# Performance work log

Hardware: AMD Instinct MI355X
Metric: run time of the kernel (lower is better)

Reference implementation:

```python
import jax, jax.numpy as jnp
import numpy as np

IN_FEATURES = 4096
OUT_FEATURES = 11008
BATCH = 2048


def setup_inputs() -> dict:
    key = jax.random.key(0)
    k1, k2, k3, k4 = jax.random.split(key, 4)
    # int8-range activations, stored as int32 for exact integer accumulation
    input = jax.random.randint(k1, (BATCH, IN_FEATURES), -127, 128, dtype=jnp.int32)
    # ternary weights in {-1, 0, 1}
    ternary_weight = jax.random.randint(k2, (OUT_FEATURES, IN_FEATURES), -1, 2, dtype=jnp.int32)
    weight_scale = jax.random.uniform(k3, (OUT_FEATURES, 1), dtype=jnp.float32, minval=0.01, maxval=0.1)
    bias = jax.random.normal(k4, (OUT_FEATURES,), dtype=jnp.float32) * 0.01
    return {"input": input, "ternary_weight": ternary_weight,
            "weight_scale": weight_scale, "bias": bias}


def reference(input, ternary_weight, weight_scale, bias):
    # Equivalent to the per-column add/sub loop: int32 accumulate of
    # input @ ternary_weight.T, since w in {-1,0,1}.
    acc = jnp.einsum('bi,oi->bo', input, ternary_weight)  # int32 [B, O]
    out = acc.astype(jnp.float32) * weight_scale.reshape(1, -1)
    out = out + bias
    return out
```

## Files before the change

### kernel.cpp

```cpp
#include <hip/hip_runtime.h>
#include <stdint.h>

#define BATCH   2048
#define KDIM    4096
#define NDIM    11008

#define BM 128
#define BN 256
#define BK 64
#define NT (KDIM / BK)
#define ABYTES (BM * BK)
#define BBYTES (BN * BK)
#define BUF_BYTES (ABYTES + BBYTES)
#define A_OFF 0
#define B_OFF ABYTES

typedef __attribute__((ext_vector_type(4))) int i32x4;

typedef const __attribute__((address_space(1))) char glob_char;
typedef __attribute__((address_space(3))) char lds_char;

__device__ __forceinline__ unsigned pack4(i32x4 v) {
  return  ((unsigned)v.x & 0xFFu)
        | (((unsigned)v.y & 0xFFu) << 8)
        | (((unsigned)v.z & 0xFFu) << 16)
        | (((unsigned)v.w)         << 24);
}

__global__ __launch_bounds__(256) void convert_i32_i8(const int* __restrict__ src,
                                                      unsigned* __restrict__ dst,
                                                      int n4) {
  int idx = blockIdx.x * 256 + threadIdx.x;
  if (idx >= n4) return;
  i32x4 v = ((const i32x4*)src)[idx];
  dst[idx] = pack4(v);
}

__global__ __launch_bounds__(256, 2) void ternary_gemm(const char* __restrict__ A8,
                                                       const char* __restrict__ B8,
                                                       const float* __restrict__ scale,
                                                       const float* __restrict__ bias,
                                                       float* __restrict__ out) {
  __shared__ char lds[3 * BUF_BYTES];

  const int tid  = threadIdx.x;
  const int wid  = tid >> 6;
  const int lane = tid & 63;

  const int nwg = gridDim.x;
  const int cpx = nwg >> 3;
  const int wg  = (blockIdx.x & 7) * cpx + (blockIdx.x >> 3);
  const int mt = wg & 15;
  const int nt = wg >> 4;
  const int arow0 = mt * BM;
  const int brow0 = nt * BN;

  const int wr = wid >> 1;
  const int wc = wid & 1;
  const int rsub = lane & 15;
  const int sgrp = lane >> 4;

  const int srow  = tid >> 2;
  const int sslot = (tid & 3) ^ ((srow >> 1) & 3);
  const char* gA0 = A8 + (size_t)(arow0       + srow) * KDIM + sslot * 16;
  const char* gA1 = A8 + (size_t)(arow0 +  64 + srow) * KDIM + sslot * 16;
  const char* gB0 = B8 + (size_t)(brow0       + srow) * KDIM + sslot * 16;
  const char* gB1 = B8 + (size_t)(brow0 +  64 + srow) * KDIM + sslot * 16;
  const char* gB2 = B8 + (size_t)(brow0 + 128 + srow) * KDIM + sslot * 16;
  const char* gB3 = B8 + (size_t)(brow0 + 192 + srow) * KDIM + sslot * 16;

  auto stage = [&](const char* g, int bufo, int kt, int dsto) {
    __builtin_amdgcn_global_load_lds((glob_char*)(g + kt * BK),
        (lds_char*)(lds + bufo + dsto + wid * 1024), 16, 0, 0);
  };

  int offA[4], offB[8];
#pragma unroll
  for (int m = 0; m < 4; ++m) {
    const int row = wr * 64 + m * 16 + rsub;
    const int p   = sgrp ^ ((row >> 1) & 3);
    offA[m] = A_OFF + row * 64 + p * 16;
  }
#pragma unroll
  for (int n = 0; n < 8; ++n) {
    const int row = wc * 128 + n * 16 + rsub;
    const int p   = sgrp ^ ((row >> 1) & 3);
    offB[n] = B_OFF + row * 64 + p * 16;
  }

  i32x4 acc[4][8];
#pragma unroll
  for (int m = 0; m < 4; ++m)
#pragma unroll
    for (int n = 0; n < 8; ++n)
      acc[m][n] = (i32x4){0, 0, 0, 0};

  int cur = 0, nxt = BUF_BYTES, pf = 2 * BUF_BYTES;

  stage(gB0, cur, 0, B_OFF);         stage(gB1, cur, 0, B_OFF + 4096);
  stage(gB2, cur, 0, B_OFF + 8192);  stage(gB3, cur, 0, B_OFF + 12288);
  stage(gA0, cur, 0, A_OFF);         stage(gA1, cur, 0, A_OFF + 4096);
  stage(gB0, nxt, 1, B_OFF);         stage(gB1, nxt, 1, B_OFF + 4096);
  stage(gB2, nxt, 1, B_OFF + 8192);  stage(gB3, nxt, 1, B_OFF + 12288);
  stage(gA0, nxt, 1, A_OFF);         stage(gA1, nxt, 1, A_OFF + 4096);
  asm volatile("s_waitcnt vmcnt(6)" ::: "memory");
  __builtin_amdgcn_s_barrier();

  for (int t = 0; t < NT; ++t) {
    const int kt2 = (t + 2 < NT) ? t + 2 : NT - 1;

    i32x4 a0, a1, a2, a3, b0, b1, b2, b3, b4, b5, b6, b7;

    a0 = *(const i32x4*)(lds + cur + offA[0]);
    a1 = *(const i32x4*)(lds + cur + offA[1]);
    b0 = *(const i32x4*)(lds + cur + offB[0]);
    b1 = *(const i32x4*)(lds + cur + offB[1]);
    b2 = *(const i32x4*)(lds + cur + offB[2]);
    b3 = *(const i32x4*)(lds + cur + offB[3]);
    stage(gB0, pf, kt2, B_OFF);
    stage(gB1, pf, kt2, B_OFF + 4096);
    __builtin_amdgcn_s_barrier();
    __builtin_amdgcn_s_setprio(1);
    acc[0][0] = __builtin_amdgcn_mfma_i32_16x16x64_i8(a0, b0, acc[0][0], 0, 0, 0);
    acc[0][1] = __builtin_amdgcn_mfma_i32_16x16x64_i8(a0, b1, acc[0][1], 0, 0, 0);
    acc[0][2] = __builtin_amdgcn_mfma_i32_16x16x64_i8(a0, b2, acc[0][2], 0, 0, 0);
    acc[0][3] = __builtin_amdgcn_mfma_i32_16x16x64_i8(a0, b3, acc[0][3], 0, 0, 0);
    acc[1][0] = __builtin_amdgcn_mfma_i32_16x16x64_i8(a1, b0, acc[1][0], 0, 0, 0);
    acc[1][1] = __builtin_amdgcn_mfma_i32_16x16x64_i8(a1, b1, acc[1][1], 0, 0, 0);
    acc[1][2] = __builtin_amdgcn_mfma_i32_16x16x64_i8(a1, b2, acc[1][2], 0, 0, 0);
    acc[1][3] = __builtin_amdgcn_mfma_i32_16x16x64_i8(a1, b3, acc[1][3], 0, 0, 0);
    __builtin_amdgcn_s_setprio(0);
    __builtin_amdgcn_s_barrier();

    b4 = *(const i32x4*)(lds + cur + offB[4]);
    b5 = *(const i32x4*)(lds + cur + offB[5]);
    b6 = *(const i32x4*)(lds + cur + offB[6]);
    b7 = *(const i32x4*)(lds + cur + offB[7]);
    stage(gB2, pf, kt2, B_OFF + 8192);
    stage(gB3, pf, kt2, B_OFF + 12288);
    __builtin_amdgcn_s_barrier();
    __builtin_amdgcn_s_setprio(1);
    acc[0][4] = __builtin_amdgcn_mfma_i32_16x16x64_i8(a0, b4, acc[0][4], 0, 0, 0);
    acc[0][5] = __builtin_amdgcn_mfma_i32_16x16x64_i8(a0, b5, acc[0][5], 0, 0, 0);
    acc[0][6] = __builtin_amdgcn_mfma_i32_16x16x64_i8(a0, b6, acc[0][6], 0, 0, 0);
    acc[0][7] = __builtin_amdgcn_mfma_i32_16x16x64_i8(a0, b7, acc[0][7], 0, 0, 0);
    acc[1][4] = __builtin_amdgcn_mfma_i32_16x16x64_i8(a1, b4, acc[1][4], 0, 0, 0);
    acc[1][5] = __builtin_amdgcn_mfma_i32_16x16x64_i8(a1, b5, acc[1][5], 0, 0, 0);
    acc[1][6] = __builtin_amdgcn_mfma_i32_16x16x64_i8(a1, b6, acc[1][6], 0, 0, 0);
    acc[1][7] = __builtin_amdgcn_mfma_i32_16x16x64_i8(a1, b7, acc[1][7], 0, 0, 0);
    __builtin_amdgcn_s_setprio(0);
    __builtin_amdgcn_s_barrier();

    a2 = *(const i32x4*)(lds + cur + offA[2]);
    a3 = *(const i32x4*)(lds + cur + offA[3]);
    stage(gA0, pf, kt2, A_OFF);
    stage(gA1, pf, kt2, A_OFF + 4096);
    __builtin_amdgcn_s_barrier();
    __builtin_amdgcn_s_setprio(1);
    acc[2][4] = __builtin_amdgcn_mfma_i32_16x16x64_i8(a2, b4, acc[2][4], 0, 0, 0);
    acc[2][5] = __builtin_amdgcn_mfma_i32_16x16x64_i8(a2, b5, acc[2][5], 0, 0, 0);
    acc[2][6] = __builtin_amdgcn_mfma_i32_16x16x64_i8(a2, b6, acc[2][6], 0, 0, 0);
    acc[2][7] = __builtin_amdgcn_mfma_i32_16x16x64_i8(a2, b7, acc[2][7], 0, 0, 0);
    acc[3][4] = __builtin_amdgcn_mfma_i32_16x16x64_i8(a3, b4, acc[3][4], 0, 0, 0);
    acc[3][5] = __builtin_amdgcn_mfma_i32_16x16x64_i8(a3, b5, acc[3][5], 0, 0, 0);
    acc[3][6] = __builtin_amdgcn_mfma_i32_16x16x64_i8(a3, b6, acc[3][6], 0, 0, 0);
    acc[3][7] = __builtin_amdgcn_mfma_i32_16x16x64_i8(a3, b7, acc[3][7], 0, 0, 0);
    __builtin_amdgcn_s_setprio(0);
    __builtin_amdgcn_s_barrier();

    asm volatile("s_waitcnt vmcnt(6)" ::: "memory");
    __builtin_amdgcn_s_barrier();
    __builtin_amdgcn_s_setprio(1);
    acc[2][0] = __builtin_amdgcn_mfma_i32_16x16x64_i8(a2, b0, acc[2][0], 0, 0, 0);
    acc[2][1] = __builtin_amdgcn_mfma_i32_16x16x64_i8(a2, b1, acc[2][1], 0, 0, 0);
    acc[2][2] = __builtin_amdgcn_mfma_i32_16x16x64_i8(a2, b2, acc[2][2], 0, 0, 0);
    acc[2][3] = __builtin_amdgcn_mfma_i32_16x16x64_i8(a2, b3, acc[2][3], 0, 0, 0);
    acc[3][0] = __builtin_amdgcn_mfma_i32_16x16x64_i8(a3, b0, acc[3][0], 0, 0, 0);
    acc[3][1] = __builtin_amdgcn_mfma_i32_16x16x64_i8(a3, b1, acc[3][1], 0, 0, 0);
    acc[3][2] = __builtin_amdgcn_mfma_i32_16x16x64_i8(a3, b2, acc[3][2], 0, 0, 0);
    acc[3][3] = __builtin_amdgcn_mfma_i32_16x16x64_i8(a3, b3, acc[3][3], 0, 0, 0);
    __builtin_amdgcn_s_setprio(0);
    __builtin_amdgcn_s_barrier();

    const int tb = cur; cur = nxt; nxt = pf; pf = tb;
  }

  const int crow = sgrp * 4;
#pragma unroll
  for (int n = 0; n < 8; ++n) {
    const int col = brow0 + wc * 128 + n * 16 + rsub;
    const float sc = scale[col];
    const float bs = bias[col];
#pragma unroll
    for (int m = 0; m < 4; ++m) {
      const int r0 = arow0 + wr * 64 + m * 16 + crow;
#pragma unroll
      for (int j = 0; j < 4; ++j) {
        out[(size_t)(r0 + j) * NDIM + col] = (float)acc[m][n][j] * sc + bs;
      }
    }
  }
}

extern "C" void kernel_launch(void* const* d_in, const int* in_sizes, int n_in,
                              void* d_out, int out_size, void* d_ws, size_t ws_size,
                              hipStream_t stream) {
  const int*   input  = (const int*)d_in[0];
  const int*   weight = (const int*)d_in[1];
  const float* scale  = (const float*)d_in[2];
  const float* bias   = (const float*)d_in[3];
  float*       out    = (float*)d_out;

  const size_t needA = (size_t)BATCH * KDIM;
  const size_t needB = (size_t)NDIM * KDIM;

  char* A8 = (char*)d_ws;
  char* B8 = A8 + needA;
  const int nA4 = (int)(needA / 4);
  const int nB4 = (int)(needB / 4);
  convert_i32_i8<<<(nA4 + 255) / 256, 256, 0, stream>>>(input, (unsigned*)A8, nA4);
  convert_i32_i8<<<(nB4 + 255) / 256, 256, 0, stream>>>(weight, (unsigned*)B8, nB4);

  const dim3 grid((BATCH / BM) * (NDIM / BN));
  const dim3 block(256);
  ternary_gemm<<<grid, block, 0, stream>>>(A8, B8, scale, bias, out);
  (void)ws_size; (void)n_in; (void)in_sizes; (void)out_size;
}
```

Measured before the change: 155.4 us.

## Flatten K-loop to single barrier phase and regroup workgroup tile mapping

```diff
diff --git a/kernel.cpp b/kernel.cpp
--- a/kernel.cpp
+++ b/kernel.cpp
@@ -47,11 +47,11 @@
   const int wid  = tid >> 6;
   const int lane = tid & 63;
 
-  const int nwg = gridDim.x;
-  const int cpx = nwg >> 3;
-  const int wg  = (blockIdx.x & 7) * cpx + (blockIdx.x >> 3);
-  const int mt = wg & 15;
-  const int nt = wg >> 4;
+  const int wg  = (blockIdx.x & 7) * 86 + (blockIdx.x >> 3);
+  const int mtq = wg / 172;
+  const int r   = wg - mtq * 172;
+  const int nt  = r >> 2;
+  const int mt  = mtq * 4 + (r & 3);
   const int arow0 = mt * BM;
   const int brow0 = nt * BN;
 
@@ -73,6 +73,14 @@
     __builtin_amdgcn_global_load_lds((glob_char*)(g + kt * BK),
         (lds_char*)(lds + bufo + dsto + wid * 1024), 16, 0, 0);
   };
+  auto stage_tile = [&](int bufo, int kt) {
+    stage(gA0, bufo, kt, A_OFF);
+    stage(gA1, bufo, kt, A_OFF + 4096);
+    stage(gB0, bufo, kt, B_OFF);
+    stage(gB1, bufo, kt, B_OFF + 4096);
+    stage(gB2, bufo, kt, B_OFF + 8192);
+    stage(gB3, bufo, kt, B_OFF + 12288);
+  };
 
   int offA[4], offB[8];
 #pragma unroll
@@ -97,89 +105,65 @@
 
   int cur = 0, nxt = BUF_BYTES, pf = 2 * BUF_BYTES;
 
-  stage(gB0, cur, 0, B_OFF);         stage(gB1, cur, 0, B_OFF + 4096);
-  stage(gB2, cur, 0, B_OFF + 8192);  stage(gB3, cur, 0, B_OFF + 12288);
-  stage(gA0, cur, 0, A_OFF);         stage(gA1, cur, 0, A_OFF + 4096);
-  stage(gB0, nxt, 1, B_OFF);         stage(gB1, nxt, 1, B_OFF + 4096);
-  stage(gB2, nxt, 1, B_OFF + 8192);  stage(gB3, nxt, 1, B_OFF + 12288);
-  stage(gA0, nxt, 1, A_OFF);         stage(gA1, nxt, 1, A_OFF + 4096);
+  stage_tile(cur, 0);
+  stage_tile(nxt, 1);
   asm volatile("s_waitcnt vmcnt(6)" ::: "memory");
   __builtin_amdgcn_s_barrier();
 
   for (int t = 0; t < NT; ++t) {
     const int kt2 = (t + 2 < NT) ? t + 2 : NT - 1;
 
-    i32x4 a0, a1, a2, a3, b0, b1, b2, b3, b4, b5, b6, b7;
-
-    a0 = *(const i32x4*)(lds + cur + offA[0]);
-    a1 = *(const i32x4*)(lds + cur + offA[1]);
-    b0 = *(const i32x4*)(lds + cur + offB[0]);
-    b1 = *(const i32x4*)(lds + cur + offB[1]);
-    b2 = *(const i32x4*)(lds + cur + offB[2]);
-    b3 = *(const i32x4*)(lds + cur + offB[3]);
-    stage(gB0, pf, kt2, B_OFF);
-    stage(gB1, pf, kt2, B_OFF + 4096);
-    __builtin_amdgcn_s_barrier();
+    stage_tile(pf, kt2);
+
+    i32x4 a0 = *(const i32x4*)(lds + cur + offA[0]);
+    i32x4 a1 = *(const i32x4*)(lds + cur + offA[1]);
+    i32x4 a2 = *(const i32x4*)(lds + cur + offA[2]);
+    i32x4 a3 = *(const i32x4*)(lds + cur + offA[3]);
+    i32x4 b0 = *(const i32x4*)(lds + cur + offB[0]);
+    i32x4 b1 = *(const i32x4*)(lds + cur + offB[1]);
+    i32x4 b2 = *(const i32x4*)(lds + cur + offB[2]);
+    i32x4 b3 = *(const i32x4*)(lds + cur + offB[3]);
+    i32x4 b4 = *(const i32x4*)(lds + cur + offB[4]);
+    i32x4 b5 = *(const i32x4*)(lds + cur + offB[5]);
+    i32x4 b6 = *(const i32x4*)(lds + cur + offB[6]);
+    i32x4 b7 = *(const i32x4*)(lds + cur + offB[7]);
+
     __builtin_amdgcn_s_setprio(1);
     acc[0][0] = __builtin_amdgcn_mfma_i32_16x16x64_i8(a0, b0, acc[0][0], 0, 0, 0);
+    acc[1][0] = __builtin_amdgcn_mfma_i32_16x16x64_i8(a1, b0, acc[1][0], 0, 0, 0);
+    acc[2][0] = __builtin_amdgcn_mfma_i32_16x16x64_i8(a2, b0, acc[2][0], 0, 0, 0);
+    acc[3][0] = __builtin_amdgcn_mfma_i32_16x16x64_i8(a3, b0, acc[3][0], 0, 0, 0);
     acc[0][1] = __builtin_amdgcn_mfma_i32_16x16x64_i8(a0, b1, acc[0][1], 0, 0, 0);
+    acc[1][1] = __builtin_amdgcn_mfma_i32_16x16x64_i8(a1, b1, acc[1][1], 0, 0, 0);
+    acc[2][1] = __builtin_amdgcn_mfma_i32_16x16x64_i8(a2, b1, acc[2][1], 0, 0, 0);
+    acc[3][1] = __builtin_amdgcn_mfma_i32_16x16x64_i8(a3, b1, acc[3][1], 0, 0, 0);
     acc[0][2] = __builtin_amdgcn_mfma_i32_16x16x64_i8(a0, b2, acc[0][2], 0, 0, 0);
+    acc[1][2] = __builtin_amdgcn_mfma_i32_16x16x64_i8(a1, b2, acc[1][2], 0, 0, 0);
+    acc[2][2] = __builtin_amdgcn_mfma_i32_16x16x64_i8(a2, b2, acc[2][2], 0, 0, 0);
+    acc[3][2] = __builtin_amdgcn_mfma_i32_16x16x64_i8(a3, b2, acc[3][2], 0, 0, 0);
     acc[0][3] = __builtin_amdgcn_mfma_i32_16x16x64_i8(a0, b3, acc[0][3], 0, 0, 0);
-    acc[1][0] = __builtin_amdgcn_mfma_i32_16x16x64_i8(a1, b0, acc[1][0], 0, 0, 0);
-    acc[1][1] = __builtin_amdgcn_mfma_i32_16x16x64_i8(a1, b1, acc[1][1], 0, 0, 0);
-    acc[1][2] = __builtin_amdgcn_mfma_i32_16x16x64_i8(a1, b2, acc[1][2], 0, 0, 0);
     acc[1][3] = __builtin_amdgcn_mfma_i32_16x16x64_i8(a1, b3, acc[1][3], 0, 0, 0);
-    __builtin_amdgcn_s_setprio(0);
-    __builtin_amdgcn_s_barrier();
-
-    b4 = *(const i32x4*)(lds + cur + offB[4]);
-    b5 = *(const i32x4*)(lds + cur + offB[5]);
-    b6 = *(const i32x4*)(lds + cur + offB[6]);
-    b7 = *(const i32x4*)(lds + cur + offB[7]);
-    stage(gB2, pf, kt2, B_OFF + 8192);
-    stage(gB3, pf, kt2, B_OFF + 12288);
-    __builtin_amdgcn_s_barrier();
-    __builtin_amdgcn_s_setprio(1);
+    acc[2][3] = __builtin_amdgcn_mfma_i32_16x16x64_i8(a2, b3, acc[2][3], 0, 0, 0);
+    acc[3][3] = __builtin_amdgcn_mfma_i32_16x16x64_i8(a3, b3, acc[3][3], 0, 0, 0);
     acc[0][4] = __builtin_amdgcn_mfma_i32_16x16x64_i8(a0, b4, acc[0][4], 0, 0, 0);
+    acc[1][4] = __builtin_amdgcn_mfma_i32_16x16x64_i8(a1, b4, acc[1][4], 0, 0, 0);
+    acc[2][4] = __builtin_amdgcn_mfma_i32_16x16x64_i8(a2, b4, acc[2][4], 0, 0, 0);
+    acc[3][4] = __builtin_amdgcn_mfma_i32_16x16x64_i8(a3, b4, acc[3][4], 0, 0, 0);
     acc[0][5] = __builtin_amdgcn_mfma_i32_16x16x64_i8(a0, b5, acc[0][5], 0, 0, 0);
+    acc[1][5] = __builtin_amdgcn_mfma_i32_16x16x64_i8(a1, b5, acc[1][5], 0, 0, 0);
+    acc[2][5] = __builtin_amdgcn_mfma_i32_16x16x64_i8(a2, b5, acc[2][5], 0, 0, 0);
+    acc[3][5] = __builtin_amdgcn_mfma_i32_16x16x64_i8(a3, b5, acc[3][5], 0, 0, 0);
     acc[0][6] = __builtin_amdgcn_mfma_i32_16x16x64_i8(a0, b6, acc[0][6], 0, 0, 0);
+    acc[1][6] = __builtin_amdgcn_mfma_i32_16x16x64_i8(a1, b6, acc[1][6], 0, 0, 0);
+    acc[2][6] = __builtin_amdgcn_mfma_i32_16x16x64_i8(a2, b6, acc[2][6], 0, 0, 0);
+    acc[3][6] = __builtin_amdgcn_mfma_i32_16x16x64_i8(a3, b6, acc[3][6], 0, 0, 0);
     acc[0][7] = __builtin_amdgcn_mfma_i32_16x16x64_i8(a0, b7, acc[0][7], 0, 0, 0);
-    acc[1][4] = __builtin_amdgcn_mfma_i32_16x16x64_i8(a1, b4, acc[1][4], 0, 0, 0);
-    acc[1][5] = __builtin_amdgcn_mfma_i32_16x16x64_i8(a1, b5, acc[1][5], 0, 0, 0);
-    acc[1][6] = __builtin_amdgcn_mfma_i32_16x16x64_i8(a1, b6, acc[1][6], 0, 0, 0);
     acc[1][7] = __builtin_amdgcn_mfma_i32_16x16x64_i8(a1, b7, acc[1][7], 0, 0, 0);
-    __builtin_amdgcn_s_setprio(0);
-    __builtin_amdgcn_s_barrier();
-
-    a2 = *(const i32x4*)(lds + cur + offA[2]);
-    a3 = *(const i32x4*)(lds + cur + offA[3]);
-    stage(gA0, pf, kt2, A_OFF);
-    stage(gA1, pf, kt2, A_OFF + 4096);
-    __builtin_amdgcn_s_barrier();
-    __builtin_amdgcn_s_setprio(1);
-    acc[2][4] = __builtin_amdgcn_mfma_i32_16x16x64_i8(a2, b4, acc[2][4], 0, 0, 0);
-    acc[2][5] = __builtin_amdgcn_mfma_i32_16x16x64_i8(a2, b5, acc[2][5], 0, 0, 0);
-    acc[2][6] = __builtin_amdgcn_mfma_i32_16x16x64_i8(a2, b6, acc[2][6], 0, 0, 0);
     acc[2][7] = __builtin_amdgcn_mfma_i32_16x16x64_i8(a2, b7, acc[2][7], 0, 0, 0);
-    acc[3][4] = __builtin_amdgcn_mfma_i32_16x16x64_i8(a3, b4, acc[3][4], 0, 0, 0);
-    acc[3][5] = __builtin_amdgcn_mfma_i32_16x16x64_i8(a3, b5, acc[3][5], 0, 0, 0);
-    acc[3][6] = __builtin_amdgcn_mfma_i32_16x16x64_i8(a3, b6, acc[3][6], 0, 0, 0);
     acc[3][7] = __builtin_amdgcn_mfma_i32_16x16x64_i8(a3, b7, acc[3][7], 0, 0, 0);
     __builtin_amdgcn_s_setprio(0);
-    __builtin_amdgcn_s_barrier();
 
     asm volatile("s_waitcnt vmcnt(6)" ::: "memory");
-    __builtin_amdgcn_s_barrier();
-    __builtin_amdgcn_s_setprio(1);
-    acc[2][0] = __builtin_amdgcn_mfma_i32_16x16x64_i8(a2, b0, acc[2][0], 0, 0, 0);
-    acc[2][1] = __builtin_amdgcn_mfma_i32_16x16x64_i8(a2, b1, acc[2][1], 0, 0, 0);
-    acc[2][2] = __builtin_amdgcn_mfma_i32_16x16x64_i8(a2, b2, acc[2][2], 0, 0, 0);
-    acc[2][3] = __builtin_amdgcn_mfma_i32_16x16x64_i8(a2, b3, acc[2][3], 0, 0, 0);
-    acc[3][0] = __builtin_amdgcn_mfma_i32_16x16x64_i8(a3, b0, acc[3][0], 0, 0, 0);
-    acc[3][1] = __builtin_amdgcn_mfma_i32_16x16x64_i8(a3, b1, acc[3][1], 0, 0, 0);
-    acc[3][2] = __builtin_amdgcn_mfma_i32_16x16x64_i8(a3, b2, acc[3][2], 0, 0, 0);
-    acc[3][3] = __builtin_amdgcn_mfma_i32_16x16x64_i8(a3, b3, acc[3][3], 0, 0, 0);
-    __builtin_amdgcn_s_setprio(0);
     __builtin_amdgcn_s_barrier();
 
     const int tb = cur; cur = nxt; nxt = pf; pf = tb;
```

Result: no change. 155.7 us (+0.2%).
